# Performance work log

Hardware: AMD Instinct MI355X
Metric: run time of the kernel (lower is better)

Reference implementation:

```python
import jax, jax.numpy as jnp
import numpy as np

IN_F, OUT_F = 2048, 2048
N_EXPERTS, RANK, TOP_K = 8, 128, 2


def setup_inputs() -> dict:
    key = jax.random.key(0)
    k_x, k_r, k_a, k_b = jax.random.split(key, 4)
    hidden_states = jax.random.normal(k_x, (4, 4096, IN_F), dtype=jnp.float32)
    # router_proj.weight is [E, in]; we store it transposed so logits = x @ router_w
    router_w = jax.random.normal(k_r, (IN_F, N_EXPERTS), dtype=jnp.float32) * (IN_F ** -0.5)
    # expert e: a_proj [in, rank], b_proj [rank, out] (transposed nn.Linear weights)
    Wa = jax.random.normal(k_a, (N_EXPERTS, IN_F, RANK), dtype=jnp.float32) * (IN_F ** -0.5)
    Wb = jax.random.normal(k_b, (N_EXPERTS, RANK, OUT_F), dtype=jnp.float32) * (RANK ** -0.5)
    return {"hidden_states": hidden_states, "router_w": router_w, "Wa": Wa, "Wb": Wb}


def reference(hidden_states, router_w, Wa, Wb):
    B, S, D = hidden_states.shape
    x = hidden_states.reshape(-1, D)  # [T, in]
    # F.normalize(x, dim=-1): x / max(||x||_2, 1e-12)
    norm = jnp.maximum(jnp.linalg.norm(x, axis=-1, keepdims=True), 1e-12)
    router_logits = (x / norm) @ router_w  # [T, E]
    routing_weights = jax.nn.softmax(router_logits.astype(jnp.float32), axis=-1)
    rw, selected_experts = jax.lax.top_k(routing_weights, TOP_K)  # [T, k]
    rw = rw / jnp.sum(rw, axis=-1, keepdims=True)
    rw = rw.astype(hidden_states.dtype)
    # combine[t, e] = routing weight if expert e selected for token t, else 0.
    combine = jnp.sum(jax.nn.one_hot(selected_experts, N_EXPERTS, dtype=rw.dtype) * rw[..., None], axis=1)  # [T, E]
    out = jnp.zeros((x.shape[0], OUT_F), dtype=hidden_states.dtype)
    for e in range(N_EXPERTS):  # small fixed expert count
        out = out + combine[:, e, None] * ((x @ Wa[e]) @ Wb[e])
    return out.reshape(B, S, OUT_F)
```

## Files before the change

kernel.cpp:

```cpp
#include <hip/hip_runtime.h>
#include <cstdint>
#include <cstddef>

#define TOKENS 16384
#define DIM    2048
#define NEXP   8
#define RANK   128
#define NOUT   2048
#define CAP    8192
#define KSL    4

typedef __attribute__((ext_vector_type(4))) float    f32x4;
typedef __attribute__((ext_vector_type(8))) _Float16 f16x8;
typedef __attribute__((ext_vector_type(4))) _Float16 f16x4;

__device__ __forceinline__ void gload_lds16(const void* g, void* l) {
  __builtin_amdgcn_global_load_lds(
      (const __attribute__((address_space(1))) void*)g,
      (__attribute__((address_space(3))) void*)l, 16, 0, 0);
}

__global__ __launch_bounds__(256) void transpose_cast_f16(
    const float* __restrict__ in, _Float16* __restrict__ out,
    int R, int C, long ostride, long obase)
{
  __shared__ float tile[32][33];
  const int e = blockIdx.z;
  const float* ine = in + (size_t)e * R * C;
  const int c0 = blockIdx.x * 32, r0 = blockIdx.y * 32;
  const int tx = threadIdx.x, ty = threadIdx.y;
#pragma unroll
  for (int j = 0; j < 32; j += 8)
    tile[ty + j][tx] = ine[(size_t)(r0 + ty + j) * C + (c0 + tx)];
  __syncthreads();
#pragma unroll
  for (int j = 0; j < 32; j += 8)
    out[(size_t)e * obase + (size_t)(c0 + ty + j) * ostride + (r0 + tx)] =
        (_Float16)tile[tx][ty + j];
}

__global__ __launch_bounds__(256) void logits_fused_kernel(
    const float* __restrict__ x, const float* __restrict__ rw,
    float* __restrict__ lgpart, float* __restrict__ ssqpart,
    _Float16* __restrict__ xh, int* __restrict__ counts)
{
  __shared__ __align__(16) char lds[65536];
  char* ldsA  = lds;
  char* ldsBh = lds + 32768;
  char* ldsBe = lds + 49152;
  const int tid = threadIdx.x;
  const int w = tid >> 6, l = tid & 63;
  const int m0 = blockIdx.x * 128;
  const int ks = blockIdx.y;
  const int kbase = ks * 512;

  if (blockIdx.x == 0 && ks == 0 && tid < 64) counts[tid] = 0;

#pragma unroll
  for (int i = 0; i < 32; ++i) {
    const int idx = tid * 32 + i;
    const int n = idx >> 9, k = idx & 511;
    const float v = (n < 8) ? rw[(size_t)(kbase + k) * 8 + n] : 0.f;
    const _Float16 h = (_Float16)v;
    const _Float16 e = (_Float16)(v - (float)h);
    const int off = n * 1024 + ((k * 2) ^ ((n & 7) << 4));
    *(_Float16*)(ldsBh + off) = h;
    *(_Float16*)(ldsBe + off) = e;
  }

  const int Lb = w * 1024 + l * 16;
  const float* agp[8];
  int ldst[8];
#pragma unroll
  for (int i = 0; i < 8; ++i) {
    const int L = i * 4096 + Lb;
    const int row = L >> 8;
    const int cb = (L & 255) ^ ((row & 7) << 4);
    agp[i] = x + (size_t)(m0 + row) * DIM + kbase + (cb >> 2);
    ldst[i] = i * 4096 + w * 1024;
  }

  f32x4 acc[2];
  float ssl[2] = {0.f, 0.f};
#pragma unroll
  for (int mf = 0; mf < 2; ++mf)
#pragma unroll
    for (int j = 0; j < 4; ++j) acc[mf][j] = 0.f;

  for (int st = 0; st < 8; ++st) {
#pragma unroll
    for (int i = 0; i < 8; ++i)
      gload_lds16(agp[i] + st * 64, ldsA + ldst[i]);
    __syncthreads();
#pragma unroll
    for (int kk = 0; kk < 2; ++kk) {
      const int n = l & 15;
      const int bko = n * 1024 +
          ((st * 128 + kk * 64 + ((l >> 4) << 4)) ^ ((n & 7) << 4));
      const f16x8 bh = *(const f16x8*)(ldsBh + bko);
      const f16x8 be = *(const f16x8*)(ldsBe + bko);
#pragma unroll
      for (int mf = 0; mf < 2; ++mf) {
        const int r = w * 32 + mf * 16 + (l & 15);
        const int s = (r & 7) << 4;
        const int c0 = kk * 128 + ((l >> 4) << 5);
        const f32x4 va = *(const f32x4*)(ldsA + r * 256 + ((c0) ^ s));
        const f32x4 vb = *(const f32x4*)(ldsA + r * 256 + ((c0 + 16) ^ s));
        float f[8] = {va[0], va[1], va[2], va[3], vb[0], vb[1], vb[2], vb[3]};
        f16x8 ah, ae;
#pragma unroll
        for (int j = 0; j < 8; ++j) {
          ah[j] = (_Float16)f[j];
          ae[j] = (_Float16)(f[j] - (float)ah[j]);
          ssl[mf] = fmaf(f[j], f[j], ssl[mf]);
        }
        *(f16x8*)(xh + (size_t)(m0 + r) * DIM + kbase + st * 64 + kk * 32 +
                  ((l >> 4) << 3)) = ah;
        acc[mf] = __builtin_amdgcn_mfma_f32_16x16x32_f16(ae, bh, acc[mf], 0, 0, 0);
        acc[mf] = __builtin_amdgcn_mfma_f32_16x16x32_f16(ah, be, acc[mf], 0, 0, 0);
        acc[mf] = __builtin_amdgcn_mfma_f32_16x16x32_f16(ah, bh, acc[mf], 0, 0, 0);
      }
    }
    __syncthreads();
  }

  const int col = l & 15;
  if (col < 8) {
#pragma unroll
    for (int mf = 0; mf < 2; ++mf) {
      const int rbase = m0 + w * 32 + mf * 16 + ((l >> 4) << 2);
#pragma unroll
      for (int j = 0; j < 4; ++j)
        lgpart[((size_t)ks * TOKENS + rbase + j) * 8 + col] = acc[mf][j];
    }
  }
#pragma unroll
  for (int mf = 0; mf < 2; ++mf) {
    float s = ssl[mf];
    s += __shfl_xor(s, 16, 64);
    s += __shfl_xor(s, 32, 64);
    if (l < 16)
      ssqpart[(size_t)ks * TOKENS + m0 + w * 32 + mf * 16 + l] = s;
  }
}

__global__ __launch_bounds__(256) void softmax_top2_kernel(
    const float* __restrict__ lgpart, const float* __restrict__ ssqpart,
    float* __restrict__ combine, int* __restrict__ counts,
    unsigned short* __restrict__ ids16)
{
  const size_t t = (size_t)blockIdx.x * 256 + threadIdx.x;
  float ss = 0.f;
  float lg[8];
#pragma unroll
  for (int e = 0; e < 8; ++e) lg[e] = 0.f;
#pragma unroll
  for (int ks = 0; ks < KSL; ++ks) {
    ss += ssqpart[(size_t)ks * TOKENS + t];
    const float* p = lgpart + ((size_t)ks * TOKENS + t) * 8;
    float4 a = *(const float4*)(p);
    float4 b = *(const float4*)(p + 4);
    lg[0] += a.x; lg[1] += a.y; lg[2] += a.z; lg[3] += a.w;
    lg[4] += b.x; lg[5] += b.y; lg[6] += b.z; lg[7] += b.w;
  }
  const float iv = 1.f / fmaxf(sqrtf(ss), 1e-12f);
#pragma unroll
  for (int e = 0; e < 8; ++e) lg[e] *= iv;
  float b1 = lg[0]; int e1 = 0;
#pragma unroll
  for (int e = 1; e < 8; ++e)
    if (lg[e] > b1) { b1 = lg[e]; e1 = e; }
  float b2 = -3.4e38f; int e2 = 0;
#pragma unroll
  for (int e = 0; e < 8; ++e)
    if (e != e1 && lg[e] > b2) { b2 = lg[e]; e2 = e; }
  const float p2 = expf(b2 - b1);
  const float w1 = 1.f / (1.f + p2);
  const float w2 = p2 * w1;
  float ov[8];
#pragma unroll
  for (int e = 0; e < 8; ++e)
    ov[e] = (e == e1) ? w1 : ((e == e2) ? w2 : 0.f);
  float4* cp = (float4*)(combine + t * 8);
  cp[0] = make_float4(ov[0], ov[1], ov[2], ov[3]);
  cp[1] = make_float4(ov[4], ov[5], ov[6], ov[7]);

  const int a = min(e1, e2), b = max(e1, e2);
  const int bin = a * 8 + b;
  const int pos = atomicAdd(&counts[bin], 1);
  if (pos < CAP) ids16[bin * CAP + pos] = (unsigned short)t;
}

__global__ void make_items_kernel(const int* __restrict__ counts,
                                  int4* __restrict__ items64,
                                  int4* __restrict__ items128)
{
  const int l = threadIdx.x;
  const int c = min(counts[l], CAP);
  const int n64 = (c + 63) >> 6;
  const int n128 = (c + 127) >> 7;
  int p64 = n64, p128 = n128;
#pragma unroll
  for (int m = 1; m < 64; m <<= 1) {
    int u = __shfl_up(p64, m, 64);  if (l >= m) p64 += u;
    int v = __shfl_up(p128, m, 64); if (l >= m) p128 += v;
  }
  const int tot64 = __shfl(p64, 63, 64);
  const int tot128 = __shfl(p128, 63, 64);
  int j = p64 - n64;
  for (int s = 0; s < c; s += 64, ++j)
    items64[j] = make_int4(l, l * CAP + s, min(64, c - s), 0);
  j = p128 - n128;
  for (int s = 0; s < c; s += 128, ++j)
    items128[j] = make_int4(l, l * CAP + s, min(128, c - s), 0);
  for (int k = tot64 + l; k < 384; k += 64) items64[k] = make_int4(-1, 0, 0, 0);
  for (int k = tot128 + l; k < 192; k += 64) items128[k] = make_int4(-1, 0, 0, 0);
}

__global__ __launch_bounds__(256) void gemm1_pair_kernel(
    const _Float16* __restrict__ xh, const _Float16* __restrict__ WaT,
    const float* __restrict__ combine, const unsigned short* __restrict__ ids,
    const int4* __restrict__ items, _Float16* __restrict__ Yc)
{
  __shared__ __align__(16) char lds[24576];
  __shared__ int ids_lds[64];
  char* ldsA = lds;
  char* ldsB = lds + 8192;
  const int4 item = items[blockIdx.y];
  if (item.x < 0) return;
  const int slot = blockIdx.x;
  const int e = slot ? (item.x & 7) : (item.x >> 3);
  const int tid = threadIdx.x;
  const int w = tid >> 6, l = tid & 63;
  const int wm = w >> 1, wn = w & 1;

  if (tid < 64)
    ids_lds[tid] = (tid < item.z) ? (int)ids[item.y + tid] : -1;
  __syncthreads();

  const int Lb = w * 1024 + l * 16;
  const _Float16* aptr[2];
  const _Float16* bptr[4];
  int ldstA[2], ldstB[4];
#pragma unroll
  for (int i = 0; i < 2; ++i) {
    const int L = i * 4096 + Lb;
    const int row = L >> 7;
    const int cb = (L & 127) ^ ((row & 7) << 4);
    int t = ids_lds[row]; if (t < 0) t = 0;
    aptr[i] = xh + (size_t)t * DIM + (cb >> 1);
    ldstA[i] = i * 4096 + w * 1024;
  }
#pragma unroll
  for (int i = 0; i < 4; ++i) {
    const int L = i * 4096 + Lb;
    const int row = L >> 7;
    const int cb = (L & 127) ^ ((row & 7) << 4);
    bptr[i] = WaT + (size_t)(e * 128 + row) * DIM + (cb >> 1);
    ldstB[i] = i * 4096 + w * 1024;
  }

  f32x4 acc[2][4];
#pragma unroll
  for (int p = 0; p < 2; ++p)
#pragma unroll
    for (int q = 0; q < 4; ++q)
#pragma unroll
      for (int j = 0; j < 4; ++j) acc[p][q][j] = 0.f;

  for (int kt = 0; kt < DIM; kt += 64) {
#pragma unroll
    for (int i = 0; i < 2; ++i)
      gload_lds16(aptr[i] + kt, ldsA + ldstA[i]);
#pragma unroll
    for (int i = 0; i < 4; ++i)
      gload_lds16(bptr[i] + kt, ldsB + ldstB[i]);
    __syncthreads();
#pragma unroll
    for (int kk = 0; kk < 2; ++kk) {
      const int kb = kk * 64 + ((l >> 4) << 4);
      f16x8 af[2], bfr[4];
#pragma unroll
      for (int mf = 0; mf < 2; ++mf) {
        const int r = (wm << 5) + (mf << 4) + (l & 15);
        af[mf] = *(const f16x8*)(ldsA + r * 128 + (kb ^ ((r & 7) << 4)));
      }
#pragma unroll
      for (int nf = 0; nf < 4; ++nf) {
        const int r = (wn << 6) + (nf << 4) + (l & 15);
        bfr[nf] = *(const f16x8*)(ldsB + r * 128 + (kb ^ ((r & 7) << 4)));
      }
#pragma unroll
      for (int mf = 0; mf < 2; ++mf)
#pragma unroll
        for (int nf = 0; nf < 4; ++nf)
          acc[mf][nf] = __builtin_amdgcn_mfma_f32_16x16x32_f16(
              af[mf], bfr[nf], acc[mf][nf], 0, 0, 0);
    }
    __syncthreads();
  }

  const int cr = (l >> 4) << 2;
  const int cc = l & 15;
#pragma unroll
  for (int mf = 0; mf < 2; ++mf) {
    const int lr0 = (wm << 5) + (mf << 4) + cr;
#pragma unroll
    for (int j = 0; j < 4; ++j) {
      const int t = ids_lds[lr0 + j];
      if (t < 0) continue;
      const float cs = combine[(size_t)t * 8 + e];
      _Float16* yr = Yc + (size_t)t * 256 + slot * 128 + (wn << 6);
#pragma unroll
      for (int nf = 0; nf < 4; ++nf)
        yr[(nf << 4) + cc] = (_Float16)(acc[mf][nf][j] * cs);
    }
  }
}

__global__ __launch_bounds__(256) void gemm2_pair_kernel(
    const _Float16* __restrict__ Y, const _Float16* __restrict__ WbT,
    const unsigned short* __restrict__ ids, const int4* __restrict__ items,
    float* __restrict__ out)
{
  __shared__ __align__(16) char lds[32768];
  __shared__ int ids_lds[128];
  char* ldsA = lds;
  char* ldsB = lds + 16384;
  const int4 item = items[blockIdx.y];
  if (item.x < 0) return;
  const int a = item.x >> 3, b = item.x & 7;
  const int n0 = blockIdx.x * 128;
  const int tid = threadIdx.x;
  const int w = tid >> 6, l = tid & 63;
  const int wm = w >> 1, wn = w & 1;

  if (tid < 128)
    ids_lds[tid] = (tid < item.z) ? (int)ids[item.y + tid] : -1;
  __syncthreads();

  const int Lb = w * 1024 + l * 16;
  const _Float16* aptr[4];
  const _Float16* bptrA[4];
  const _Float16* bptrB[4];
  int ldst[4];
#pragma unroll
  for (int i = 0; i < 4; ++i) {
    const int L = i * 4096 + Lb;
    const int row = L >> 7;
    const int cb = (L & 127) ^ ((row & 7) << 4);
    int t = ids_lds[row]; if (t < 0) t = 0;
    aptr[i]  = Y + (size_t)t * 256 + (cb >> 1);
    bptrA[i] = WbT + (size_t)(n0 + row) * 1024 + a * 128 + (cb >> 1);
    bptrB[i] = WbT + (size_t)(n0 + row) * 1024 + b * 128 + (cb >> 1);
    ldst[i] = i * 4096 + w * 1024;
  }

  f32x4 acc[4][4];
#pragma unroll
  for (int p = 0; p < 4; ++p)
#pragma unroll
    for (int q = 0; q < 4; ++q)
#pragma unroll
      for (int j = 0; j < 4; ++j) acc[p][q][j] = 0.f;

#pragma unroll
  for (int kt = 0; kt < 4; ++kt) {
#pragma unroll
    for (int i = 0; i < 4; ++i) {
      gload_lds16(aptr[i] + kt * 64, ldsA + ldst[i]);
      const _Float16* bs = (kt < 2) ? (bptrA[i] + kt * 64)
                                    : (bptrB[i] + (kt - 2) * 64);
      gload_lds16(bs, ldsB + ldst[i]);
    }
    __syncthreads();
#pragma unroll
    for (int kk = 0; kk < 2; ++kk) {
      const int kb = kk * 64 + ((l >> 4) << 4);
      f16x8 af[4], bfr[4];
#pragma unroll
      for (int mf = 0; mf < 4; ++mf) {
        const int r = (wm << 6) + (mf << 4) + (l & 15);
        af[mf] = *(const f16x8*)(ldsA + r * 128 + (kb ^ ((r & 7) << 4)));
      }
#pragma unroll
      for (int nf = 0; nf < 4; ++nf) {
        const int r = (wn << 6) + (nf << 4) + (l & 15);
        bfr[nf] = *(const f16x8*)(ldsB + r * 128 + (kb ^ ((r & 7) << 4)));
      }
#pragma unroll
      for (int mf = 0; mf < 4; ++mf)
#pragma unroll
        for (int nf = 0; nf < 4; ++nf)
          acc[mf][nf] = __builtin_amdgcn_mfma_f32_16x16x32_f16(
              af[mf], bfr[nf], acc[mf][nf], 0, 0, 0);
    }
    __syncthreads();
  }

  const int cr = (l >> 4) << 2;
  const int cc = l & 15;
#pragma unroll
  for (int mf = 0; mf < 4; ++mf) {
    const int lr0 = (wm << 6) + (mf << 4) + cr;
#pragma unroll
    for (int j = 0; j < 4; ++j) {
      const int t = ids_lds[lr0 + j];
      if (t < 0) continue;
      float* orow = out + (size_t)t * NOUT + n0;
#pragma unroll
      for (int nf = 0; nf < 4; ++nf)
        orow[(wn << 6) + (nf << 4) + cc] = acc[mf][nf][j];
    }
  }
}

extern "C" void kernel_launch(void* const* d_in, const int* in_sizes, int n_in,
                              void* d_out, int out_size, void* d_ws, size_t ws_size,
                              hipStream_t stream) {
  const float* x  = (const float*)d_in[0];
  const float* rw = (const float*)d_in[1];
  const float* Wa = (const float*)d_in[2];
  const float* Wb = (const float*)d_in[3];
  float* out = (float*)d_out;

  char* ws = (char*)d_ws;
  _Float16* xh       = (_Float16*)(ws);
  _Float16* WaT      = (_Float16*)(ws + 67108864);
  _Float16* WbT      = (_Float16*)(ws + 71303168);
  float*    combine  = (float*)   (ws + 75497472);
  int*      counts   = (int*)     (ws + 76021760);
  int4*     items64  = (int4*)    (ws + 76022016);
  int4*     items128 = (int4*)    (ws + 76028160);
  unsigned short* ids16 = (unsigned short*)(ws + 76031232);
  _Float16* Yc       = (_Float16*)(ws + 77079808);
  float*    lgpart   = (float*)   (ws + 77079808);
  float*    ssqpart  = (float*)   (ws + 79177728);

  transpose_cast_f16<<<dim3(4, 64, 8), dim3(32, 8), 0, stream>>>(
      Wa, WaT, 2048, 128, 2048, (long)128 * 2048);
  transpose_cast_f16<<<dim3(64, 4, 8), dim3(32, 8), 0, stream>>>(
      Wb, WbT, 128, 2048, 1024, 128);

  logits_fused_kernel<<<dim3(TOKENS / 128, KSL), 256, 0, stream>>>(
      x, rw, lgpart, ssqpart, xh, counts);

  softmax_top2_kernel<<<TOKENS / 256, 256, 0, stream>>>(
      lgpart, ssqpart, combine, counts, ids16);
  make_items_kernel<<<1, 64, 0, stream>>>(counts, items64, items128);

  gemm1_pair_kernel<<<dim3(2, 384), 256, 0, stream>>>(
      xh, WaT, combine, ids16, items64, Yc);
  gemm2_pair_kernel<<<dim3(NOUT / 128, 192), 256, 0, stream>>>(
      Yc, WbT, ids16, items128, out);
}
```

Measured before the change: 181.2 us.

## Fuse both experts of a pair into one gemm1 block with 32-token tiles

gemm1 previously launched two blocks per 64-token item, one per expert slot, each loading the same gathered token rows. Now one block handles a 32-token tile against both experts' Wa slices (256 output columns), so the gathered x rows are loaded once and shared by the two experts. Each wave owns 64 columns across all 32 rows. This halves the per-block M tile, raises per-block B traffic and LDS use (36KB), and changes item count and workspace offsets.

Measured after the change: 190.9 us. +5.3%, slower.

```diff
diff --git a/kernel.cpp b/kernel.cpp
--- a/kernel.cpp
+++ b/kernel.cpp
@@ -192,28 +192,28 @@
 }
 
 __global__ void make_items_kernel(const int* __restrict__ counts,
-                                  int4* __restrict__ items64,
+                                  int4* __restrict__ items32,
                                   int4* __restrict__ items128)
 {
   const int l = threadIdx.x;
   const int c = min(counts[l], CAP);
-  const int n64 = (c + 63) >> 6;
+  const int n32 = (c + 31) >> 5;
   const int n128 = (c + 127) >> 7;
-  int p64 = n64, p128 = n128;
+  int p32 = n32, p128 = n128;
 #pragma unroll
   for (int m = 1; m < 64; m <<= 1) {
-    int u = __shfl_up(p64, m, 64);  if (l >= m) p64 += u;
+    int u = __shfl_up(p32, m, 64);  if (l >= m) p32 += u;
     int v = __shfl_up(p128, m, 64); if (l >= m) p128 += v;
   }
-  const int tot64 = __shfl(p64, 63, 64);
+  const int tot32 = __shfl(p32, 63, 64);
   const int tot128 = __shfl(p128, 63, 64);
-  int j = p64 - n64;
-  for (int s = 0; s < c; s += 64, ++j)
-    items64[j] = make_int4(l, l * CAP + s, min(64, c - s), 0);
+  int j = p32 - n32;
+  for (int s = 0; s < c; s += 32, ++j)
+    items32[j] = make_int4(l, l * CAP + s, min(32, c - s), 0);
   j = p128 - n128;
   for (int s = 0; s < c; s += 128, ++j)
     items128[j] = make_int4(l, l * CAP + s, min(128, c - s), 0);
-  for (int k = tot64 + l; k < 384; k += 64) items64[k] = make_int4(-1, 0, 0, 0);
+  for (int k = tot32 + l; k < 576; k += 64) items32[k] = make_int4(-1, 0, 0, 0);
   for (int k = tot128 + l; k < 192; k += 64) items128[k] = make_int4(-1, 0, 0, 0);
 }
 
@@ -222,42 +222,36 @@
     const float* __restrict__ combine, const unsigned short* __restrict__ ids,
     const int4* __restrict__ items, _Float16* __restrict__ Yc)
 {
-  __shared__ __align__(16) char lds[24576];
-  __shared__ int ids_lds[64];
+  __shared__ __align__(16) char lds[36864];
+  __shared__ int ids_lds[32];
   char* ldsA = lds;
-  char* ldsB = lds + 8192;
-  const int4 item = items[blockIdx.y];
+  char* ldsB = lds + 4096;
+  const int4 item = items[blockIdx.x];
   if (item.x < 0) return;
-  const int slot = blockIdx.x;
-  const int e = slot ? (item.x & 7) : (item.x >> 3);
+  const int ea = item.x >> 3, eb = item.x & 7;
   const int tid = threadIdx.x;
   const int w = tid >> 6, l = tid & 63;
-  const int wm = w >> 1, wn = w & 1;
-
-  if (tid < 64)
+
+  if (tid < 32)
     ids_lds[tid] = (tid < item.z) ? (int)ids[item.y + tid] : -1;
   __syncthreads();
 
-  const int Lb = w * 1024 + l * 16;
-  const _Float16* aptr[2];
-  const _Float16* bptr[4];
-  int ldstA[2], ldstB[4];
-#pragma unroll
-  for (int i = 0; i < 2; ++i) {
-    const int L = i * 4096 + Lb;
+  const int arow = tid >> 3;
+  const int acb = (((tid & 7) << 4) ^ ((arow & 7) << 4));
+  int ta = ids_lds[arow]; if (ta < 0) ta = 0;
+  const _Float16* aptr = xh + (size_t)ta * DIM + (acb >> 1);
+  const int aoff = tid * 16;
+
+  const _Float16* bptr[8];
+  int boff[8];
+#pragma unroll
+  for (int i = 0; i < 8; ++i) {
+    const int L = i * 4096 + tid * 16;
     const int row = L >> 7;
     const int cb = (L & 127) ^ ((row & 7) << 4);
-    int t = ids_lds[row]; if (t < 0) t = 0;
-    aptr[i] = xh + (size_t)t * DIM + (cb >> 1);
-    ldstA[i] = i * 4096 + w * 1024;
-  }
-#pragma unroll
-  for (int i = 0; i < 4; ++i) {
-    const int L = i * 4096 + Lb;
-    const int row = L >> 7;
-    const int cb = (L & 127) ^ ((row & 7) << 4);
-    bptr[i] = WaT + (size_t)(e * 128 + row) * DIM + (cb >> 1);
-    ldstB[i] = i * 4096 + w * 1024;
+    const int e = (row < 128) ? ea : eb;
+    bptr[i] = WaT + (size_t)(e * 128 + (row & 127)) * DIM + (cb >> 1);
+    boff[i] = L;
   }
 
   f32x4 acc[2][4];
@@ -269,12 +263,10 @@
       for (int j = 0; j < 4; ++j) acc[p][q][j] = 0.f;
 
   for (int kt = 0; kt < DIM; kt += 64) {
-#pragma unroll
-    for (int i = 0; i < 2; ++i)
-      gload_lds16(aptr[i] + kt, ldsA + ldstA[i]);
-#pragma unroll
-    for (int i = 0; i < 4; ++i)
-      gload_lds16(bptr[i] + kt, ldsB + ldstB[i]);
+    gload_lds16(aptr + kt, ldsA + aoff);
+#pragma unroll
+    for (int i = 0; i < 8; ++i)
+      gload_lds16(bptr[i] + kt, ldsB + boff[i]);
     __syncthreads();
 #pragma unroll
     for (int kk = 0; kk < 2; ++kk) {
@@ -282,12 +274,12 @@
       f16x8 af[2], bfr[4];
 #pragma unroll
       for (int mf = 0; mf < 2; ++mf) {
-        const int r = (wm << 5) + (mf << 4) + (l & 15);
+        const int r = (mf << 4) + (l & 15);
         af[mf] = *(const f16x8*)(ldsA + r * 128 + (kb ^ ((r & 7) << 4)));
       }
 #pragma unroll
       for (int nf = 0; nf < 4; ++nf) {
-        const int r = (wn << 6) + (nf << 4) + (l & 15);
+        const int r = (w << 6) + (nf << 4) + (l & 15);
         bfr[nf] = *(const f16x8*)(ldsB + r * 128 + (kb ^ ((r & 7) << 4)));
       }
 #pragma unroll
@@ -300,17 +292,19 @@
     __syncthreads();
   }
 
+  const int e_sel = (w < 2) ? ea : eb;
+  const int slot = w >> 1;
   const int cr = (l >> 4) << 2;
   const int cc = l & 15;
 #pragma unroll
   for (int mf = 0; mf < 2; ++mf) {
-    const int lr0 = (wm << 5) + (mf << 4) + cr;
+    const int lr0 = (mf << 4) + cr;
 #pragma unroll
     for (int j = 0; j < 4; ++j) {
       const int t = ids_lds[lr0 + j];
       if (t < 0) continue;
-      const float cs = combine[(size_t)t * 8 + e];
-      _Float16* yr = Yc + (size_t)t * 256 + slot * 128 + (wn << 6);
+      const float cs = combine[(size_t)t * 8 + e_sel];
+      _Float16* yr = Yc + (size_t)t * 256 + slot * 128 + ((w & 1) << 6);
 #pragma unroll
       for (int nf = 0; nf < 4; ++nf)
         yr[(nf << 4) + cc] = (_Float16)(acc[mf][nf][j] * cs);
@@ -430,12 +424,12 @@
   _Float16* WbT      = (_Float16*)(ws + 71303168);
   float*    combine  = (float*)   (ws + 75497472);
   int*      counts   = (int*)     (ws + 76021760);
-  int4*     items64  = (int4*)    (ws + 76022016);
-  int4*     items128 = (int4*)    (ws + 76028160);
-  unsigned short* ids16 = (unsigned short*)(ws + 76031232);
-  _Float16* Yc       = (_Float16*)(ws + 77079808);
-  float*    lgpart   = (float*)   (ws + 77079808);
-  float*    ssqpart  = (float*)   (ws + 79177728);
+  int4*     items32  = (int4*)    (ws + 76022016);
+  int4*     items128 = (int4*)    (ws + 76031232);
+  unsigned short* ids16 = (unsigned short*)(ws + 76034304);
+  _Float16* Yc       = (_Float16*)(ws + 77082880);
+  float*    lgpart   = (float*)   (ws + 77082880);
+  float*    ssqpart  = (float*)   (ws + 79180032);
 
   transpose_cast_f16<<<dim3(4, 64, 8), dim3(32, 8), 0, stream>>>(
       Wa, WaT, 2048, 128, 2048, (long)128 * 2048);
@@ -447,10 +441,10 @@
 
   softmax_top2_kernel<<<TOKENS / 256, 256, 0, stream>>>(
       lgpart, ssqpart, combine, counts, ids16);
-  make_items_kernel<<<1, 64, 0, stream>>>(counts, items64, items128);
-
-  gemm1_pair_kernel<<<dim3(2, 384), 256, 0, stream>>>(
-      xh, WaT, combine, ids16, items64, Yc);
+  make_items_kernel<<<1, 64, 0, stream>>>(counts, items32, items128);
+
+  gemm1_pair_kernel<<<576, 256, 0, stream>>>(
+      xh, WaT, combine, ids16, items32, Yc);
   gemm2_pair_kernel<<<dim3(NOUT / 128, 192), 256, 0, stream>>>(
       Yc, WbT, ids16, items128, out);
 }
```
